# Kernel optimization log

Measured on AMD Instinct MI355X. Metric: run time of the kernel, lower is better.

Reference implementation:

```python
import jax, jax.numpy as jnp
import numpy as np

B, T, D, H = 2, 2048, 1024, 16
HD = D // H  # 64


def setup_inputs() -> dict:
    key = jax.random.key(0)
    ks = jax.random.split(key, 9)
    s = 1.0 / np.sqrt(D)
    return {
        "x": jax.random.normal(ks[0], (B, T, D), dtype=jnp.float32),
        "Wq": jax.random.uniform(ks[1], (D, D), minval=-s, maxval=s, dtype=jnp.float32),
        "bq": jax.random.uniform(ks[2], (D,), minval=-s, maxval=s, dtype=jnp.float32),
        "Wk": jax.random.uniform(ks[3], (D, D), minval=-s, maxval=s, dtype=jnp.float32),
        "bk": jax.random.uniform(ks[4], (D,), minval=-s, maxval=s, dtype=jnp.float32),
        "Wv": jax.random.uniform(ks[5], (D, D), minval=-s, maxval=s, dtype=jnp.float32),
        "bv": jax.random.uniform(ks[6], (D,), minval=-s, maxval=s, dtype=jnp.float32),
        "Wo": jax.random.uniform(ks[7], (D, D), minval=-s, maxval=s, dtype=jnp.float32),
        "bo": jax.random.uniform(ks[8], (D,), minval=-s, maxval=s, dtype=jnp.float32),
    }


def reference(x, Wq, bq, Wk, bk, Wv, bv, Wo, bo):
    b, t, d = x.shape
    # projections (nn.Linear: x @ W.T + b), split heads -> [B,H,T,hd]
    def split_heads(y):
        return y.reshape(b, t, H, HD).transpose(0, 2, 1, 3)
    Q = split_heads(x @ Wq.T + bq)
    K = split_heads(x @ Wk.T + bk)
    V = split_heads(x @ Wv.T + bv)
    # causal linear attention via cumulative outer-product state
    # Z[b,h,s,p,n] = V[b,h,s,p] * K[b,h,s,n]
    Z = jnp.einsum('bhsp,bhsn->bhspn', V, K)
    Z_cum = jnp.cumsum(Z, axis=2)  # prefix sum over time -> causal state
    Y = jnp.einsum('bhtn,bhtpn->bhtp', Q, Z_cum)  # [B,H,T,hd]
    Y = Y.transpose(0, 2, 1, 3).reshape(b, t, d)
    return Y @ Wo.T + bo
```

## Files before the change

### kernel.cpp

```cpp
#include <hip/hip_runtime.h>
#include <stdint.h>

#define B_  2
#define T_  2048
#define D_  1024
#define H_  16
#define HD_ 64
#define M_  (B_*T_)
#define CHK 128
#define NC  (T_/CHK)
#define BH  (B_*H_)

#define XN   4194304
#define WN   1048576

typedef unsigned short ushort_t;
typedef unsigned int   uint_t;

typedef __bf16 bf16x8 __attribute__((ext_vector_type(8)));
typedef float  f32x4  __attribute__((ext_vector_type(4)));

__device__ inline ushort_t f2bf(float f) {
    uint_t x = __float_as_uint(f);
    x += 0x7fffu + ((x >> 16) & 1u);
    return (ushort_t)(x >> 16);
}
__device__ inline float lo_bf(uint_t u) { return __uint_as_float(u << 16); }
__device__ inline float hi_bf(uint_t u) { return __uint_as_float(u & 0xffff0000u); }

__device__ inline uint4 pack8(const float4& lo, const float4& hi) {
    uint4 pk;
    pk.x = (uint_t)f2bf(lo.x) | ((uint_t)f2bf(lo.y) << 16);
    pk.y = (uint_t)f2bf(lo.z) | ((uint_t)f2bf(lo.w) << 16);
    pk.z = (uint_t)f2bf(hi.x) | ((uint_t)f2bf(hi.y) << 16);
    pk.w = (uint_t)f2bf(hi.z) | ((uint_t)f2bf(hi.w) << 16);
    return pk;
}

__global__ __launch_bounds__(256) void to_bf16_all(
    const float* __restrict__ x,  const float* __restrict__ Wq,
    const float* __restrict__ Wk, const float* __restrict__ Wv,
    const float* __restrict__ Wo, ushort_t* __restrict__ dst)
{
    const int idx = blockIdx.x * 256 + threadIdx.x;
    const int e   = idx * 8;
    const float* src;
    if      (e < XN)          src = x  + e;
    else if (e < XN + WN)     src = Wq + (e - XN);
    else if (e < XN + 2*WN)   src = Wk + (e - XN - WN);
    else if (e < XN + 3*WN)   src = Wv + (e - XN - 2*WN);
    else                      src = Wo + (e - XN - 3*WN);
    float4 lo = ((const float4*)src)[0];
    float4 hi = ((const float4*)src)[1];
    *(uint4*)(dst + e) = pack8(lo, hi);
}

__device__ inline void stage32(const ushort_t* __restrict__ g, ushort_t* ldsw, int lane) {
    const int rr  = lane >> 3;
    const int kg8 = ((lane & 7) ^ rr) << 3;
    const ushort_t* src = g + (size_t)rr * D_ + kg8;
    #pragma unroll
    for (int i = 0; i < 4; i++) {
        __builtin_amdgcn_global_load_lds(
            (const __attribute__((address_space(1))) void*)(src + (size_t)(i * 8) * D_),
            (__attribute__((address_space(3))) void*)(ldsw + i * 512),
            16, 0, 0);
    }
}

__global__ __launch_bounds__(256) void gemm_qkv(
    const ushort_t* __restrict__ xb, const ushort_t* __restrict__ Wqkvb,
    const float* __restrict__ bq, const float* __restrict__ bk,
    const float* __restrict__ bv, ushort_t* __restrict__ qkv_ws)
{
    const int z = blockIdx.z;
    const ushort_t* W  = Wqkvb + (size_t)z * WN;
    const float*    bi = (z == 0) ? bq : ((z == 1) ? bk : bv);
    ushort_t* out = qkv_ws + (size_t)z * (size_t)M_ * D_;

    __shared__ __align__(16) ushort_t As[128 * 64];
    __shared__ __align__(16) ushort_t Bs[128 * 64];

    const int tid  = threadIdx.x;
    const int m0   = blockIdx.y * 128;
    const int n0   = blockIdx.x * 128;
    const int wave = tid >> 6;
    const int lane = tid & 63;
    const int wm   = (wave >> 1) * 64;
    const int wn   = (wave & 1) * 64;
    const int fr   = lane & 15;
    const int quad = lane >> 4;

    const ushort_t* Ag = xb + (size_t)(m0 + wave * 32) * D_;
    const ushort_t* Bg = W  + (size_t)(n0 + wave * 32) * D_;
    ushort_t* Alds = &As[wave * 32 * 64];
    ushort_t* Blds = &Bs[wave * 32 * 64];

    f32x4 acc[4][4];
    #pragma unroll
    for (int i = 0; i < 4; i++)
        #pragma unroll
        for (int j = 0; j < 4; j++)
            acc[i][j] = (f32x4){0.f, 0.f, 0.f, 0.f};

    for (int k0 = 0; k0 < D_; k0 += 64) {
        __syncthreads();
        stage32(Ag + k0, Alds, lane);
        stage32(Bg + k0, Blds, lane);
        __syncthreads();

        #pragma unroll
        for (int ksg = 0; ksg <= 4; ksg += 4) {
            const int kgo = ((ksg + quad) ^ (fr & 7)) << 3;
            bf16x8 af[4], bf[4];
            #pragma unroll
            for (int i = 0; i < 4; i++) {
                uint4 u = *(const uint4*)&As[(wm + i * 16 + fr) * 64 + kgo];
                af[i] = __builtin_bit_cast(bf16x8, u);
            }
            #pragma unroll
            for (int j = 0; j < 4; j++) {
                uint4 u = *(const uint4*)&Bs[(wn + j * 16 + fr) * 64 + kgo];
                bf[j] = __builtin_bit_cast(bf16x8, u);
            }
            #pragma unroll
            for (int i = 0; i < 4; i++)
                #pragma unroll
                for (int j = 0; j < 4; j++)
                    acc[i][j] = __builtin_amdgcn_mfma_f32_16x16x32_bf16(
                        af[i], bf[j], acc[i][j], 0, 0, 0);
        }
    }

    const int rb = quad * 4;
    #pragma unroll
    for (int j = 0; j < 4; j++) {
        const int n = n0 + wn + j * 16 + fr;
        const float bias = bi[n];
        const int h  = n >> 6;
        const int hd = n & 63;
        #pragma unroll
        for (int i = 0; i < 4; i++) {
            #pragma unroll
            for (int r = 0; r < 4; r++) {
                const int m = m0 + wm + i * 16 + rb + r;
                const int b = m >> 11, t = m & (T_ - 1);
                out[(((size_t)(b * H_ + h)) * T_ + t) * HD_ + hd] =
                    f2bf(acc[i][j][r] + bias);
            }
        }
    }
}

__global__ __launch_bounds__(256) void gemm_out(
    const ushort_t* __restrict__ Yw, const ushort_t* __restrict__ Wob,
    const float* __restrict__ bo, float* __restrict__ out)
{
    __shared__ __align__(16) ushort_t As[128 * 64];
    __shared__ __align__(16) ushort_t Bs[128 * 64];

    const int tid  = threadIdx.x;
    const int m0   = blockIdx.y * 128;
    const int n0   = blockIdx.x * 128;
    const int wave = tid >> 6;
    const int lane = tid & 63;
    const int wm   = (wave >> 1) * 64;
    const int wn   = (wave & 1) * 64;
    const int fr   = lane & 15;
    const int quad = lane >> 4;

    const ushort_t* Ag = Yw  + (size_t)(m0 + wave * 32) * D_;
    const ushort_t* Bg = Wob + (size_t)(n0 + wave * 32) * D_;
    ushort_t* Alds = &As[wave * 32 * 64];
    ushort_t* Blds = &Bs[wave * 32 * 64];

    f32x4 acc[4][4];
    #pragma unroll
    for (int i = 0; i < 4; i++)
        #pragma unroll
        for (int j = 0; j < 4; j++)
            acc[i][j] = (f32x4){0.f, 0.f, 0.f, 0.f};

    for (int k0 = 0; k0 < D_; k0 += 64) {
        __syncthreads();
        stage32(Ag + k0, Alds, lane);
        stage32(Bg + k0, Blds, lane);
        __syncthreads();

        #pragma unroll
        for (int ksg = 0; ksg <= 4; ksg += 4) {
            const int kgo = ((ksg + quad) ^ (fr & 7)) << 3;
            bf16x8 af[4], bf[4];
            #pragma unroll
            for (int i = 0; i < 4; i++) {
                uint4 u = *(const uint4*)&As[(wm + i * 16 + fr) * 64 + kgo];
                af[i] = __builtin_bit_cast(bf16x8, u);
            }
            #pragma unroll
            for (int j = 0; j < 4; j++) {
                uint4 u = *(const uint4*)&Bs[(wn + j * 16 + fr) * 64 + kgo];
                bf[j] = __builtin_bit_cast(bf16x8, u);
            }
            #pragma unroll
            for (int i = 0; i < 4; i++)
                #pragma unroll
                for (int j = 0; j < 4; j++)
                    acc[i][j] = __builtin_amdgcn_mfma_f32_16x16x32_bf16(
                        af[i], bf[j], acc[i][j], 0, 0, 0);
        }
    }

    const int rb = quad * 4;
    #pragma unroll
    for (int j = 0; j < 4; j++) {
        const int n = n0 + wn + j * 16 + fr;
        const float bias = bo[n];
        #pragma unroll
        for (int i = 0; i < 4; i++) {
            #pragma unroll
            for (int r = 0; r < 4; r++) {
                const int m = m0 + wm + i * 16 + rb + r;
                out[(size_t)m * D_ + n] = acc[i][j][r] + bias;
            }
        }
    }
}

#define LDS_ 136

__device__ inline void stage_T(const ushort_t* __restrict__ src, ushort_t* dst, int tid) {
    #pragma unroll
    for (int g = 0; g < 4; g++) {
        const int v  = tid + 256 * g;
        const int s  = v >> 3;
        const int p8 = (v & 7) * 8;
        uint4 u = ((const uint4*)src)[v];
        ushort_t e[8];
        *(uint4*)e = u;
        const int sb = s >> 3, slo = s & 7;
        #pragma unroll
        for (int j = 0; j < 8; j++) {
            const int p   = p8 + j;
            const int blk = (sb & 8) | ((sb ^ (p >> 3)) & 7);
            dst[p * LDS_ + (blk << 3) + slo] = e[j];
        }
    }
}

__global__ __launch_bounds__(256) void chunk_delta(
    const ushort_t* __restrict__ k_ws, const ushort_t* __restrict__ v_ws,
    float* __restrict__ deltas)
{
    const int c = blockIdx.x, bh = blockIdx.y;
    __shared__ __align__(16) ushort_t VtS[64 * LDS_];
    __shared__ __align__(16) ushort_t KtS[64 * LDS_];
    const int tid = threadIdx.x;
    const int wave = tid >> 6, lane = tid & 63;
    const int fr = lane & 15, quad = lane >> 4, rb = quad * 4;
    const size_t base = ((size_t)bh * T_ + (size_t)c * CHK) * HD_;

    stage_T(v_ws + base, VtS, tid);
    stage_T(k_ws + base, KtS, tid);
    __syncthreads();

    const int p = wave * 16 + fr;
    f32x4 acc[4];
    #pragma unroll
    for (int jn = 0; jn < 4; jn++) acc[jn] = (f32x4){0.f, 0.f, 0.f, 0.f};

    #pragma unroll
    for (int kt = 0; kt < 4; kt++) {
        const int sb   = kt * 4 + quad;
        const int blkA = (sb & 8) | ((sb ^ (p >> 3)) & 7);
        bf16x8 af = __builtin_bit_cast(bf16x8, *(const uint4*)&VtS[p * LDS_ + (blkA << 3)]);
        #pragma unroll
        for (int jn = 0; jn < 4; jn++) {
            const int n    = jn * 16 + fr;
            const int blkB = (sb & 8) | ((sb ^ (n >> 3)) & 7);
            uint4 ub = *(const uint4*)&KtS[n * LDS_ + (blkB << 3)];
            acc[jn] = __builtin_amdgcn_mfma_f32_16x16x32_bf16(
                af, __builtin_bit_cast(bf16x8, ub), acc[jn], 0, 0, 0);
        }
    }

    float* dp = deltas + ((size_t)bh * NC + c) * 4096;
    #pragma unroll
    for (int jn = 0; jn < 4; jn++)
        #pragma unroll
        for (int r = 0; r < 4; r++)
            dp[(wave * 16 + rb + r) * 64 + jn * 16 + fr] = acc[jn][r];
}

__global__ __launch_bounds__(256) void prefix_states(
    const float* __restrict__ deltas, ushort_t* __restrict__ states_bf)
{
    const int bh = blockIdx.x, tid = threadIdx.x;
    float acc[16];
    #pragma unroll
    for (int j = 0; j < 16; j++) acc[j] = 0.f;
    for (int c = 0; c < NC; c++) {
        const float* dp = deltas    + ((size_t)bh * NC + c) * 4096;
        ushort_t*    sp = states_bf + ((size_t)bh * NC + c) * 4096;
        #pragma unroll
        for (int j = 0; j < 16; j++) {
            const int e = j * 256 + tid;
            sp[e] = f2bf(acc[j]);
            acc[j] += dp[e];
        }
    }
}

__global__ __launch_bounds__(256) void attn_chunk(
    const ushort_t* __restrict__ q_ws, const ushort_t* __restrict__ k_ws,
    const ushort_t* __restrict__ v_ws, const ushort_t* __restrict__ states_bf,
    ushort_t* __restrict__ y_ws)
{
    const int c = blockIdx.x, bh = blockIdx.y;
    __shared__ __align__(16) ushort_t VtS[64 * LDS_];
    __shared__ __align__(16) ushort_t Smat[128 * LDS_];

    const int tid  = threadIdx.x;
    const int wave = tid >> 6;
    const int lane = tid & 63;
    const int fr   = lane & 15;
    const int quad = lane >> 4;
    const int fk   = quad * 8;
    const int rb   = quad * 4;

    const size_t base = ((size_t)bh * T_ + (size_t)c * CHK) * HD_;
    const ushort_t* qg = q_ws + base;
    const ushort_t* kg = k_ws + base;
    const ushort_t* vg = v_ws + base;
    const ushort_t* st = states_bf + ((size_t)bh * NC + c) * 4096;

    stage_T(vg, VtS, tid);
    __syncthreads();

    const int mt[2] = { wave, 7 - wave };

    bf16x8 aq[2][2];
    #pragma unroll
    for (int i = 0; i < 2; i++)
        #pragma unroll
        for (int kk = 0; kk < 2; kk++) {
            uint4 u = *(const uint4*)(qg + (mt[i] * 16 + fr) * HD_ + kk * 32 + fk);
            aq[i][kk] = __builtin_bit_cast(bf16x8, u);
        }

    f32x4 acc[2][4];
    #pragma unroll
    for (int i = 0; i < 2; i++)
        #pragma unroll
        for (int jn = 0; jn < 4; jn++)
            acc[i][jn] = (f32x4){0.f, 0.f, 0.f, 0.f};

    #pragma unroll
    for (int jn = 0; jn < 4; jn++) {
        #pragma unroll
        for (int kk = 0; kk < 2; kk++) {
            uint4 u = *(const uint4*)(st + (jn * 16 + fr) * 64 + kk * 32 + fk);
            bf16x8 bsp = __builtin_bit_cast(bf16x8, u);
            #pragma unroll
            for (int i = 0; i < 2; i++)
                acc[i][jn] = __builtin_amdgcn_mfma_f32_16x16x32_bf16(
                    aq[i][kk], bsp, acc[i][jn], 0, 0, 0);
        }
    }

    #pragma unroll
    for (int i = 0; i < 2; i++) {
        const int m  = mt[i];
        const int nk = (m + 2) >> 1;
        const int jt = 2 * nk;

        f32x4 sc[8];
        #pragma unroll
        for (int j = 0; j < 8; j++) sc[j] = (f32x4){0.f, 0.f, 0.f, 0.f};

        #pragma unroll
        for (int j = 0; j < 8; j++) {
            if (j <= m) {
                #pragma unroll
                for (int kk = 0; kk < 2; kk++) {
                    uint4 u = *(const uint4*)(kg + (j * 16 + fr) * HD_ + kk * 32 + fk);
                    sc[j] = __builtin_amdgcn_mfma_f32_16x16x32_bf16(
                        aq[i][kk], __builtin_bit_cast(bf16x8, u), sc[j], 0, 0, 0);
                }
            }
        }

        #pragma unroll
        for (int j = 0; j < 8; j++) {
            if (j < jt) {
                f32x4 v = sc[j];
                if (j == m) {
                    #pragma unroll
                    for (int r = 0; r < 4; r++)
                        if (fr > rb + r) v[r] = 0.f;
                }
                #pragma unroll
                for (int r = 0; r < 4; r++)
                    Smat[(m * 16 + rb + r) * LDS_ + j * 16 + fr] = f2bf(v[r]);
            }
        }

        #pragma unroll
        for (int kt = 0; kt < 4; kt++) {
            if (kt < nk) {
                uint4 ua = *(const uint4*)&Smat[(m * 16 + fr) * LDS_ + kt * 32 + fk];
                bf16x8 as_ = __builtin_bit_cast(bf16x8, ua);
                #pragma unroll
                for (int jn = 0; jn < 4; jn++) {
                    const int p   = jn * 16 + fr;
                    const int sb  = kt * 4 + quad;
                    const int blk = (sb & 8) | ((sb ^ (p >> 3)) & 7);
                    uint4 ub = *(const uint4*)&VtS[p * LDS_ + (blk << 3)];
                    acc[i][jn] = __builtin_amdgcn_mfma_f32_16x16x32_bf16(
                        as_, __builtin_bit_cast(bf16x8, ub), acc[i][jn], 0, 0, 0);
                }
            }
        }
    }

    const int b = bh >> 4, h = bh & 15;
    ushort_t* yg = y_ws + ((size_t)(b * T_ + c * CHK)) * D_ + h * 64;
    #pragma unroll
    for (int i = 0; i < 2; i++) {
        #pragma unroll
        for (int jn = 0; jn < 4; jn++) {
            #pragma unroll
            for (int r = 0; r < 4; r++) {
                const int t = mt[i] * 16 + rb + r;
                const int p = jn * 16 + fr;
                yg[(size_t)t * D_ + p] = f2bf(acc[i][jn][r]);
            }
        }
    }
}

extern "C" void kernel_launch(void* const* d_in, const int* in_sizes, int n_in,
                              void* d_out, int out_size, void* d_ws, size_t ws_size,
                              hipStream_t stream)
{
    const float* x  = (const float*)d_in[0];
    const float* Wq = (const float*)d_in[1];
    const float* bq = (const float*)d_in[2];
    const float* Wk = (const float*)d_in[3];
    const float* bk = (const float*)d_in[4];
    const float* Wv = (const float*)d_in[5];
    const float* bv = (const float*)d_in[6];
    const float* Wo = (const float*)d_in[7];
    const float* bo = (const float*)d_in[8];
    float* out = (float*)d_out;

    ushort_t* cvt    = (ushort_t*)d_ws;
    ushort_t* xb     = cvt;
    ushort_t* Wqkvb  = cvt + (size_t)XN;
    ushort_t* Wob    = cvt + (size_t)XN + 3 * WN;
    ushort_t* q_ws   = cvt + (size_t)XN + 4 * WN;
    ushort_t* k_ws   = q_ws + (size_t)M_ * D_;
    ushort_t* v_ws   = k_ws + (size_t)M_ * D_;
    ushort_t* y_ws   = v_ws + (size_t)M_ * D_;
    float*    deltas    = (float*)xb;
    ushort_t* states_bf = Wqkvb;

    to_bf16_all<<<dim3((XN + 4 * WN) / 8 / 256), 256, 0, stream>>>(
        x, Wq, Wk, Wv, Wo, cvt);
    gemm_qkv<<<dim3(D_ / 128, M_ / 128, 3), 256, 0, stream>>>(
        xb, Wqkvb, bq, bk, bv, q_ws);
    chunk_delta<<<dim3(NC, BH), 256, 0, stream>>>(k_ws, v_ws, deltas);
    prefix_states<<<dim3(BH), 256, 0, stream>>>(deltas, states_bf);
    attn_chunk<<<dim3(NC, BH), 256, 0, stream>>>(q_ws, k_ws, v_ws, states_bf, y_ws);
    gemm_out<<<dim3(D_ / 128, M_ / 128), 256, 0, stream>>>(y_ws, Wob, bo, out);
}
```

Baseline: 191.0 us.

## Fuse chunk delta and prefix-scan kernels into one sequential per-head state kernel

```diff
diff --git a/kernel.cpp b/kernel.cpp
--- a/kernel.cpp
+++ b/kernel.cpp
@@ -228,15 +228,14 @@
 
 #define LDS_ 136
 
-__device__ inline void stage_T(const ushort_t* __restrict__ src, ushort_t* dst, int tid) {
+__device__ inline void scatter_T(const uint4* u, ushort_t* dst, int tid) {
     #pragma unroll
     for (int g = 0; g < 4; g++) {
         const int v  = tid + 256 * g;
         const int s  = v >> 3;
         const int p8 = (v & 7) * 8;
-        uint4 u = ((const uint4*)src)[v];
         ushort_t e[8];
-        *(uint4*)e = u;
+        *(uint4*)e = u[g];
         const int sb = s >> 3, slo = s & 7;
         #pragma unroll
         for (int j = 0; j < 8; j++) {
@@ -247,65 +246,76 @@
     }
 }
 
-__global__ __launch_bounds__(256) void chunk_delta(
+__device__ inline void stage_T(const ushort_t* __restrict__ src, ushort_t* dst, int tid) {
+    uint4 u[4];
+    #pragma unroll
+    for (int g = 0; g < 4; g++) u[g] = ((const uint4*)src)[tid + 256 * g];
+    scatter_T(u, dst, tid);
+}
+
+__global__ __launch_bounds__(256) void chunk_states(
     const ushort_t* __restrict__ k_ws, const ushort_t* __restrict__ v_ws,
-    float* __restrict__ deltas)
-{
-    const int c = blockIdx.x, bh = blockIdx.y;
-    __shared__ __align__(16) ushort_t VtS[64 * LDS_];
-    __shared__ __align__(16) ushort_t KtS[64 * LDS_];
-    const int tid = threadIdx.x;
+    ushort_t* __restrict__ states_bf)
+{
+    const int bh = blockIdx.x;
+    __shared__ __align__(16) ushort_t KtS[2][64 * LDS_];
+    __shared__ __align__(16) ushort_t VtS[2][64 * LDS_];
+
+    const int tid  = threadIdx.x;
     const int wave = tid >> 6, lane = tid & 63;
     const int fr = lane & 15, quad = lane >> 4, rb = quad * 4;
-    const size_t base = ((size_t)bh * T_ + (size_t)c * CHK) * HD_;
-
-    stage_T(v_ws + base, VtS, tid);
-    stage_T(k_ws + base, KtS, tid);
-    __syncthreads();
-
-    const int p = wave * 16 + fr;
-    f32x4 acc[4];
-    #pragma unroll
-    for (int jn = 0; jn < 4; jn++) acc[jn] = (f32x4){0.f, 0.f, 0.f, 0.f};
-
-    #pragma unroll
-    for (int kt = 0; kt < 4; kt++) {
-        const int sb   = kt * 4 + quad;
-        const int blkA = (sb & 8) | ((sb ^ (p >> 3)) & 7);
-        bf16x8 af = __builtin_bit_cast(bf16x8, *(const uint4*)&VtS[p * LDS_ + (blkA << 3)]);
-        #pragma unroll
-        for (int jn = 0; jn < 4; jn++) {
-            const int n    = jn * 16 + fr;
-            const int blkB = (sb & 8) | ((sb ^ (n >> 3)) & 7);
-            uint4 ub = *(const uint4*)&KtS[n * LDS_ + (blkB << 3)];
-            acc[jn] = __builtin_amdgcn_mfma_f32_16x16x32_bf16(
-                af, __builtin_bit_cast(bf16x8, ub), acc[jn], 0, 0, 0);
-        }
-    }
-
-    float* dp = deltas + ((size_t)bh * NC + c) * 4096;
-    #pragma unroll
-    for (int jn = 0; jn < 4; jn++)
-        #pragma unroll
-        for (int r = 0; r < 4; r++)
-            dp[(wave * 16 + rb + r) * 64 + jn * 16 + fr] = acc[jn][r];
-}
-
-__global__ __launch_bounds__(256) void prefix_states(
-    const float* __restrict__ deltas, ushort_t* __restrict__ states_bf)
-{
-    const int bh = blockIdx.x, tid = threadIdx.x;
-    float acc[16];
-    #pragma unroll
-    for (int j = 0; j < 16; j++) acc[j] = 0.f;
+    const int p  = wave * 16 + fr;
+
+    const uint4* kp = (const uint4*)(k_ws + (size_t)bh * T_ * HD_);
+    const uint4* vp = (const uint4*)(v_ws + (size_t)bh * T_ * HD_);
+
+    uint4 kv[4], vv[4];
+    #pragma unroll
+    for (int g = 0; g < 4; g++) {
+        kv[g] = kp[tid + 256 * g];
+        vv[g] = vp[tid + 256 * g];
+    }
+
+    f32x4 accs[4];
+    #pragma unroll
+    for (int jn = 0; jn < 4; jn++) accs[jn] = (f32x4){0.f, 0.f, 0.f, 0.f};
+
     for (int c = 0; c < NC; c++) {
-        const float* dp = deltas    + ((size_t)bh * NC + c) * 4096;
-        ushort_t*    sp = states_bf + ((size_t)bh * NC + c) * 4096;
-        #pragma unroll
-        for (int j = 0; j < 16; j++) {
-            const int e = j * 256 + tid;
-            sp[e] = f2bf(acc[j]);
-            acc[j] += dp[e];
+        const int buf = c & 1;
+        scatter_T(kv, KtS[buf], tid);
+        scatter_T(vv, VtS[buf], tid);
+        __syncthreads();
+
+        if (c + 1 < NC) {
+            const int off = (c + 1) * 1024;
+            #pragma unroll
+            for (int g = 0; g < 4; g++) {
+                kv[g] = kp[off + tid + 256 * g];
+                vv[g] = vp[off + tid + 256 * g];
+            }
+        }
+
+        ushort_t* sp = states_bf + ((size_t)bh * NC + c) * 4096;
+        #pragma unroll
+        for (int jn = 0; jn < 4; jn++)
+            #pragma unroll
+            for (int r = 0; r < 4; r++)
+                sp[(wave * 16 + rb + r) * 64 + jn * 16 + fr] = f2bf(accs[jn][r]);
+
+        #pragma unroll
+        for (int kt = 0; kt < 4; kt++) {
+            const int sb   = kt * 4 + quad;
+            const int blkA = (sb & 8) | ((sb ^ (p >> 3)) & 7);
+            bf16x8 af = __builtin_bit_cast(bf16x8,
+                *(const uint4*)&VtS[buf][p * LDS_ + (blkA << 3)]);
+            #pragma unroll
+            for (int jn = 0; jn < 4; jn++) {
+                const int n    = jn * 16 + fr;
+                const int blkB = (sb & 8) | ((sb ^ (n >> 3)) & 7);
+                uint4 ub = *(const uint4*)&KtS[buf][n * LDS_ + (blkB << 3)];
+                accs[jn] = __builtin_amdgcn_mfma_f32_16x16x32_bf16(
+                    af, __builtin_bit_cast(bf16x8, ub), accs[jn], 0, 0, 0);
+            }
         }
     }
 }
@@ -461,15 +471,13 @@
     ushort_t* k_ws   = q_ws + (size_t)M_ * D_;
     ushort_t* v_ws   = k_ws + (size_t)M_ * D_;
     ushort_t* y_ws   = v_ws + (size_t)M_ * D_;
-    float*    deltas    = (float*)xb;
     ushort_t* states_bf = Wqkvb;
 
     to_bf16_all<<<dim3((XN + 4 * WN) / 8 / 256), 256, 0, stream>>>(
         x, Wq, Wk, Wv, Wo, cvt);
     gemm_qkv<<<dim3(D_ / 128, M_ / 128, 3), 256, 0, stream>>>(
         xb, Wqkvb, bq, bk, bv, q_ws);
-    chunk_delta<<<dim3(NC, BH), 256, 0, stream>>>(k_ws, v_ws, deltas);
-    prefix_states<<<dim3(BH), 256, 0, stream>>>(deltas, states_bf);
+    chunk_states<<<dim3(BH), 256, 0, stream>>>(k_ws, v_ws, states_bf);
     attn_chunk<<<dim3(NC, BH), 256, 0, stream>>>(q_ws, k_ws, v_ws, states_bf, y_ws);
     gemm_out<<<dim3(D_ / 128, M_ / 128), 256, 0, stream>>>(y_ws, Wob, bo, out);
 }
```

New measurement: 195.4 us. 2.3% more time.
